# Optimization experiments

Measured on AMD Instinct MI355X. Metric: run time of the kernel, lower is better.

## Reference

```python
import jax, jax.numpy as jnp
import numpy as np

B, N, M = 2, 10000, 320000
F, LAT, STY = 64, 128, 128
HEADS, HID = 4, 32
OUT = 3 + F  # 67
NEG = 0.2    # leaky relu slope (both activation and GAT attention)
EPS = 1e-5


def leaky(x):
    return jax.nn.leaky_relu(x, NEG)


def layer_norm(x, g, b):
    mu = jnp.mean(x, axis=-1, keepdims=True)
    var = jnp.var(x, axis=-1, keepdims=True)
    return (x - mu) * jax.lax.rsqrt(var + EPS) * g + b


def gat_conv(h, src, dst, W, a_src, a_dst, bias, heads, out_dim, n_nodes, concat):
    # h: [n, in]; W: [in, heads*out_dim]; a_*: [heads, out_dim]
    ht = (h @ W).reshape(n_nodes, heads, out_dim)
    al_s = jnp.einsum('nhd,hd->nh', ht, a_src)  # source contribution
    al_d = jnp.einsum('nhd,hd->nh', ht, a_dst)  # destination contribution
    e = leaky(al_s[src] + al_d[dst])            # [E, heads]
    emax = jax.ops.segment_max(e, dst, num_segments=n_nodes)
    ex = jnp.exp(e - emax[dst])
    denom = jax.ops.segment_sum(ex, dst, num_segments=n_nodes)
    alpha = ex / (denom[dst] + 1e-16)           # scatter-softmax over in-edges
    msg = ht[src] * alpha[:, :, None]           # [E, heads, out_dim]
    agg = jax.ops.segment_sum(msg, dst, num_segments=n_nodes)
    agg = agg.reshape(n_nodes, heads * out_dim) if concat else agg.mean(axis=1)
    return agg + bias


def setup_inputs():
    key = jax.random.key(0)
    ks = jax.random.split(key, 20)
    g = lambda i, sh, s=0.05: jax.random.normal(ks[i], sh, jnp.float32) * s
    d = {}
    d['z'] = g(0, (B, LAT), 1.0)
    d['x'] = g(1, (N, F), 1.0)
    d['pos'] = g(2, (N, 3), 1.0)
    d['edge_index'] = jax.random.randint(ks[3], (2, M), 0, N)
    d['w1'] = g(4, (LAT, 256)); d['b1'] = jnp.zeros((256,), jnp.float32)
    d['w2'] = g(5, (256, 512)); d['b2'] = jnp.zeros((512,), jnp.float32)
    d['w3'] = g(6, (512, STY)); d['b3'] = jnp.zeros((STY,), jnp.float32)
    in0 = F + STY
    d['gw0'] = g(7, (in0, HEADS * HID)); d['ga0s'] = g(8, (HEADS, HID)); d['ga0d'] = g(9, (HEADS, HID)); d['gb0'] = jnp.zeros((HEADS * HID,), jnp.float32)
    in1 = HEADS * HID
    d['gw1'] = g(10, (in1, HEADS * HID)); d['ga1s'] = g(11, (HEADS, HID)); d['ga1d'] = g(12, (HEADS, HID)); d['gb1'] = jnp.zeros((HEADS * HID,), jnp.float32)
    d['gw2'] = g(13, (in1, OUT)); d['ga2s'] = g(14, (1, OUT)); d['ga2d'] = g(15, (1, OUT)); d['gb2'] = jnp.zeros((OUT,), jnp.float32)
    d['ln0_g'] = jnp.ones((in1,), jnp.float32); d['ln0_b'] = jnp.zeros((in1,), jnp.float32)
    d['ln1_g'] = jnp.ones((in1,), jnp.float32); d['ln1_b'] = jnp.zeros((in1,), jnp.float32)
    return d


def _batched_edges(edge_index):
    # replicate template edges B times with node-id offsets, then add self-loops
    ei = jnp.concatenate([edge_index + b * N for b in range(B)], axis=1)
    sl = jnp.arange(B * N, dtype=edge_index.dtype)
    src = jnp.concatenate([ei[0], sl])
    dst = jnp.concatenate([ei[1], sl])
    return src, dst


def _forward(z, x, pos, src, dst,
             w1, b1, w2, b2, w3, b3,
             gw0, ga0s, ga0d, gb0, gw1, ga1s, ga1d, gb1, gw2, ga2s, ga2d, gb2,
             ln0_g, ln0_b, ln1_g, ln1_b):
    n_tot = B * N
    # style MLP
    s = leaky(z @ w1 + b1)
    s = leaky(s @ w2 + b2)
    style = s @ w3 + b3                               # [B, STY]
    xb = jnp.tile(x, (B, 1))                          # [B*N, F]
    pb = jnp.tile(pos, (B, 1))                        # [B*N, 3]
    style_exp = jnp.repeat(style, N, axis=0)          # [B*N, STY]
    H = jnp.concatenate([xb, style_exp], axis=1)
    H = gat_conv(H, src, dst, gw0, ga0s, ga0d, gb0, HEADS, HID, n_tot, True)
    H = leaky(layer_norm(H, ln0_g, ln0_b))
    H = gat_conv(H, src, dst, gw1, ga1s, ga1d, gb1, HEADS, HID, n_tot, True)
    H = leaky(layer_norm(H, ln1_g, ln1_b))
    H_out = gat_conv(H, src, dst, gw2, ga2s, ga2d, gb2, 1, OUT, n_tot, False)
    p_new = pb + H_out[:, :3]
    f_new = xb + H_out[:, 3:]
    return f_new, p_new


def reference(z, x, pos, edge_index,
              w1, b1, w2, b2, w3, b3,
              gw0, ga0s, ga0d, gb0, gw1, ga1s, ga1d, gb1, gw2, ga2s, ga2d, gb2,
              ln0_g, ln0_b, ln1_g, ln1_b):
    src, dst = _batched_edges(edge_index)
    return _forward(z, x, pos, src, dst,
                    w1, b1, w2, b2, w3, b3,
                    gw0, ga0s, ga0d, gb0, gw1, ga1s, ga1d, gb1, gw2, ga2s, ga2d, gb2,
                    ln0_g, ln0_b, ln1_g, ln1_b)
```

## Files before the change

### kernel.cpp

```cpp
#include <hip/hip_runtime.h>
#include <hip/hip_bf16.h>

#define DEV_INLINE __device__ __forceinline__

constexpr int Nn   = 10000;
constexpr int NT   = 20000;
constexpr int Me   = 320000;
constexpr int STRIDE = 96;
constexpr float NEG = 0.2f;

typedef float  f32x4  __attribute__((ext_vector_type(4)));
typedef short  bf16x8 __attribute__((ext_vector_type(8)));

DEV_INLINE float leaky(float x){ return x >= 0.f ? x : NEG*x; }

DEV_INLINE ushort f2bf(float v){
  __hip_bfloat16 h = __float2bfloat16(v);
  return *reinterpret_cast<ushort*>(&h);
}
DEV_INLINE float bf2f(ushort u){
  uint x = ((uint)u) << 16;
  return __uint_as_float(x);
}
DEV_INLINE float sel4(float4 w, int h){
  return h < 2 ? (h == 0 ? w.x : w.y) : (h == 2 ? w.z : w.w);
}
DEV_INLINE float red16(float v){
  v += __shfl_xor(v, 1); v += __shfl_xor(v, 2);
  v += __shfl_xor(v, 4); v += __shfl_xor(v, 8);
  return v;
}
DEV_INLINE float red32(float v){
  v += __shfl_xor(v, 1); v += __shfl_xor(v, 2);
  v += __shfl_xor(v, 4); v += __shfl_xor(v, 8);
  v += __shfl_xor(v, 16);
  return v;
}

template<int K>
__global__ __launch_bounds__(256) void k_mlp(const float* __restrict__ in,
    const float* __restrict__ W, const float* __restrict__ bias,
    float* __restrict__ out, int OD, int doAct, int mlpBlocks,
    int* __restrict__ zbuf, int zn, int zblk,
    const float* __restrict__ xsrc, ushort* __restrict__ xdst, int xn4){
  if ((int)blockIdx.x >= mlpBlocks){
    int b2 = blockIdx.x - mlpBlocks;
    if (b2 < zblk){
      int i = b2*256 + threadIdx.x;
      if (i < zn) zbuf[i] = 0;
    } else {
      int i4 = (b2 - zblk)*256 + threadIdx.x;
      if (i4 < xn4){
        float4 v = ((const float4*)xsrc)[i4];
        ushort4 o;
        o.x = f2bf(v.x); o.y = f2bf(v.y); o.z = f2bf(v.z); o.w = f2bf(v.w);
        ((ushort4*)xdst)[i4] = o;
      }
    }
    return;
  }
  int wave = threadIdx.x >> 6, lane = threadIdx.x & 63;
  int o = blockIdx.x*4 + wave;
  if (o >= 2*OD) return;
  int b = (o >= OD) ? 1 : 0;
  int j = o - b*OD;
  const float* __restrict__ ip = in + b*K;
  float acc = 0.f;
  #pragma unroll 2
  for (int k = lane; k < K; k += 64) acc += ip[k] * W[(size_t)k*OD + j];
  #pragma unroll
  for (int off = 32; off; off >>= 1) acc += __shfl_xor(acc, off);
  if (lane == 0){
    float v = acc + (bias ? bias[j] : 0.f);
    out[o] = doAct ? leaky(v) : v;
  }
}

__global__ __launch_bounds__(256) void k_ht0_mfma(const ushort* __restrict__ xb,
    const float* __restrict__ gw0, const float* __restrict__ styleW0,
    const float* __restrict__ a_s, const float* __restrict__ a_d,
    ushort* __restrict__ ht0, float* __restrict__ alS, float* __restrict__ alD,
    int mbBlocks, const int* __restrict__ eidx, int* __restrict__ cnt,
    ushort* __restrict__ slot){
  if ((int)blockIdx.x >= mbBlocks){
    int e = (blockIdx.x - mbBlocks)*256 + threadIdx.x;
    if (e < Me){
      int s = eidx[e], d = eidx[Me + e];
      int p = atomicAdd(&cnt[d], 1);
      if (p < STRIDE) slot[(size_t)d*STRIDE + p] = (ushort)s;
    }
    return;
  }
  __shared__ ushort bt[128*64];
  __shared__ float stycS[2][4], stycD[2][4];
  int t = threadIdx.x;
  int wid = t >> 6, lane = t & 63, l15 = lane & 15, g = lane >> 4;
  int mbase = blockIdx.x*128 + wid*32;

  bf16x8 afr[2][2];
  #pragma unroll
  for (int mf=0; mf<2; mf++){
    int row = mbase + mf*16 + l15;
    int rc = row < Nn ? row : Nn-1;
    const ushort* ap = xb + (size_t)rc*64 + g*8;
    #pragma unroll
    for (int ks=0; ks<2; ks++)
      afr[mf][ks] = *(const bf16x8*)(ap + ks*32);
  }

  for (int idx = t; idx < 64*128; idx += 256){
    int k = idx >> 7, c = idx & 127;
    uint byte = ((uint)(c*64 + k) << 1) ^ ((uint)(c&7) << 4);
    *(ushort*)((char*)bt + byte) = f2bf(gw0[k*128 + c]);
  }

  if (t < 128){
    int c = t, h = c >> 5;
    float as_c = a_s[c], ad_c = a_d[c];
    float s0 = styleW0[c], s1 = styleW0[128 + c];
    float v0s = red32(s0*as_c), v0d = red32(s0*ad_c);
    float v1s = red32(s1*as_c), v1d = red32(s1*ad_c);
    if ((lane & 31) == 0){
      stycS[0][h] = v0s; stycD[0][h] = v0d;
      stycS[1][h] = v1s; stycD[1][h] = v1d;
    }
  }
  __syncthreads();

  f32x4 acc[2][8];
  #pragma unroll
  for (int mf=0; mf<2; mf++)
    #pragma unroll
    for (int nf=0; nf<8; nf++) acc[mf][nf] = (f32x4){0.f,0.f,0.f,0.f};

  #pragma unroll
  for (int ks=0; ks<2; ks++){
    int kb = ks*32 + g*8;
    bf16x8 bfr[8];
    #pragma unroll
    for (int nf=0; nf<8; nf++){
      int c = nf*16 + l15;
      uint byte = ((uint)(c*64 + kb) << 1) ^ ((uint)(c&7) << 4);
      bfr[nf] = *(const bf16x8*)((const char*)bt + byte);
    }
    #pragma unroll
    for (int mf=0; mf<2; mf++)
      #pragma unroll
      for (int nf=0; nf<8; nf++)
        acc[mf][nf] = __builtin_amdgcn_mfma_f32_16x16x32_bf16(
            afr[mf][ks], bfr[nf], acc[mf][nf], 0, 0, 0);
  }

  float sw0[8], sw1[8], as_v[8], ad_v[8];
  #pragma unroll
  for (int nf=0; nf<8; nf++){
    int c = nf*16 + l15;
    sw0[nf] = styleW0[c]; sw1[nf] = styleW0[128 + c];
    as_v[nf] = a_s[c];    ad_v[nf] = a_d[c];
  }
  #pragma unroll
  for (int mf=0; mf<2; mf++){
    int rbase = mbase + mf*16 + g*4;
    #pragma unroll
    for (int r=0; r<4; r++){
      int row = rbase + r;
      bool ok = (row < Nn);
      #pragma unroll
      for (int nf=0; nf<8; nf++){
        int c = nf*16 + l15;
        if (ok){
          float v = acc[mf][nf][r];
          ht0[(size_t)row*128 + c]      = f2bf(v + sw0[nf]);
          ht0[(size_t)(Nn+row)*128 + c] = f2bf(v + sw1[nf]);
        }
      }
      float ps0 = acc[mf][0][r]*as_v[0] + acc[mf][1][r]*as_v[1];
      float ps1 = acc[mf][2][r]*as_v[2] + acc[mf][3][r]*as_v[3];
      float ps2 = acc[mf][4][r]*as_v[4] + acc[mf][5][r]*as_v[5];
      float ps3 = acc[mf][6][r]*as_v[6] + acc[mf][7][r]*as_v[7];
      float pd0 = acc[mf][0][r]*ad_v[0] + acc[mf][1][r]*ad_v[1];
      float pd1 = acc[mf][2][r]*ad_v[2] + acc[mf][3][r]*ad_v[3];
      float pd2 = acc[mf][4][r]*ad_v[4] + acc[mf][5][r]*ad_v[5];
      float pd3 = acc[mf][6][r]*ad_v[6] + acc[mf][7][r]*ad_v[7];
      ps0 = red16(ps0); ps1 = red16(ps1); ps2 = red16(ps2); ps3 = red16(ps3);
      pd0 = red16(pd0); pd1 = red16(pd1); pd2 = red16(pd2); pd3 = red16(pd3);
      if (l15 == 0 && ok){
        *(float4*)(alS + (size_t)row*4) = make_float4(
            ps0 + stycS[0][0], ps1 + stycS[0][1], ps2 + stycS[0][2], ps3 + stycS[0][3]);
        *(float4*)(alD + (size_t)row*4) = make_float4(
            pd0 + stycD[0][0], pd1 + stycD[0][1], pd2 + stycD[0][2], pd3 + stycD[0][3]);
        *(float4*)(alS + (size_t)(Nn+row)*4) = make_float4(
            ps0 + stycS[1][0], ps1 + stycS[1][1], ps2 + stycS[1][2], ps3 + stycS[1][3]);
        *(float4*)(alD + (size_t)(Nn+row)*4) = make_float4(
            pd0 + stycD[1][0], pd1 + stycD[1][1], pd2 + stycD[1][2], pd3 + stycD[1][3]);
      }
    }
  }
}

template<int NCOL, int LDO, int NF, int NHEAD>
__global__ __launch_bounds__(256) void k_mm_mfma(const ushort* __restrict__ A,
    const float* __restrict__ W, ushort* __restrict__ out,
    const float* __restrict__ a_s, const float* __restrict__ a_d,
    float* __restrict__ alS, float* __restrict__ alD, int M){
  constexpr int NCOLP = NF*16;
  __shared__ ushort bt[NCOLP*128];
  int t = threadIdx.x;
  int wid = t >> 6, lane = t & 63, l15 = lane & 15, g = lane >> 4;
  int mbase = blockIdx.x*128 + wid*32;

  bf16x8 afr[2][4];
  #pragma unroll
  for (int mf=0; mf<2; mf++){
    int row = mbase + mf*16 + l15;
    int rc = row < M ? row : M-1;
    const ushort* ap = A + (size_t)rc*128 + g*8;
    #pragma unroll
    for (int ks=0; ks<4; ks++)
      afr[mf][ks] = *(const bf16x8*)(ap + ks*32);
  }

  for (int idx = t; idx < 128*NCOLP; idx += 256){
    int k = idx / NCOLP, c = idx % NCOLP;
    float v = (c < NCOL) ? W[k*NCOL + c] : 0.f;
    uint byte = ((uint)(c*128 + k) << 1) ^ ((uint)(c&7) << 4);
    *(ushort*)((char*)bt + byte) = f2bf(v);
  }
  __syncthreads();

  f32x4 acc[2][NF];
  #pragma unroll
  for (int mf=0; mf<2; mf++)
    #pragma unroll
    for (int nf=0; nf<NF; nf++) acc[mf][nf] = (f32x4){0.f,0.f,0.f,0.f};

  #pragma unroll
  for (int ks=0; ks<4; ks++){
    int kb = ks*32 + g*8;
    bf16x8 bfr[NF];
    #pragma unroll
    for (int nf=0; nf<NF; nf++){
      int c = nf*16 + l15;
      uint byte = ((uint)(c*128 + kb) << 1) ^ ((uint)(c&7) << 4);
      bfr[nf] = *(const bf16x8*)((const char*)bt + byte);
    }
    #pragma unroll
    for (int mf=0; mf<2; mf++)
      #pragma unroll
      for (int nf=0; nf<NF; nf++)
        acc[mf][nf] = __builtin_amdgcn_mfma_f32_16x16x32_bf16(
            afr[mf][ks], bfr[nf], acc[mf][nf], 0, 0, 0);
  }

  #pragma unroll
  for (int mf=0; mf<2; mf++){
    int rbase = mbase + mf*16 + g*4;
    #pragma unroll
    for (int nf=0; nf<NF; nf++){
      int c = nf*16 + l15;
      if (c < LDO){
        #pragma unroll
        for (int r=0; r<4; r++){
          int row = rbase + r;
          if (row < M) out[(size_t)row*LDO + c] = (c < NCOL) ? f2bf(acc[mf][nf][r]) : (ushort)0;
        }
      }
    }
  }

  float as_v[NF], ad_v[NF];
  #pragma unroll
  for (int nf=0; nf<NF; nf++){
    int c = nf*16 + l15;
    as_v[nf] = (c < NCOL) ? a_s[c] : 0.f;
    ad_v[nf] = (c < NCOL) ? a_d[c] : 0.f;
  }
  #pragma unroll
  for (int mf=0; mf<2; mf++){
    #pragma unroll
    for (int r=0; r<4; r++){
      int row = mbase + mf*16 + g*4 + r;
      if (NHEAD == 4){
        float ps0 = acc[mf][0][r]*as_v[0] + acc[mf][1][r]*as_v[1];
        float ps1 = acc[mf][2][r]*as_v[2] + acc[mf][3][r]*as_v[3];
        float ps2 = acc[mf][4][r]*as_v[4] + acc[mf][5][r]*as_v[5];
        float ps3 = acc[mf][6][r]*as_v[6] + acc[mf][7][r]*as_v[7];
        float pd0 = acc[mf][0][r]*ad_v[0] + acc[mf][1][r]*ad_v[1];
        float pd1 = acc[mf][2][r]*ad_v[2] + acc[mf][3][r]*ad_v[3];
        float pd2 = acc[mf][4][r]*ad_v[4] + acc[mf][5][r]*ad_v[5];
        float pd3 = acc[mf][6][r]*ad_v[6] + acc[mf][7][r]*ad_v[7];
        ps0 = red16(ps0); ps1 = red16(ps1); ps2 = red16(ps2); ps3 = red16(ps3);
        pd0 = red16(pd0); pd1 = red16(pd1); pd2 = red16(pd2); pd3 = red16(pd3);
        if (l15 == 0 && row < M){
          *(float4*)(alS + (size_t)row*4) = make_float4(ps0, ps1, ps2, ps3);
          *(float4*)(alD + (size_t)row*4) = make_float4(pd0, pd1, pd2, pd3);
        }
      } else {
        float ps = 0.f, pd = 0.f;
        #pragma unroll
        for (int nf=0; nf<NF; nf++){
          ps += acc[mf][nf][r]*as_v[nf];
          pd += acc[mf][nf][r]*ad_v[nf];
        }
        ps = red16(ps); pd = red16(pd);
        if (l15 == 0 && row < M){
          alS[row] = ps; alD[row] = pd;
        }
      }
    }
  }
}

__global__ __launch_bounds__(256) void k_gat128(const ushort* __restrict__ ht,
    const float* __restrict__ alS, const float* __restrict__ alD,
    const int* __restrict__ deg, const ushort* __restrict__ slot,
    const float* __restrict__ gb, const float* __restrict__ lng,
    const float* __restrict__ lnb, ushort* __restrict__ outH, int n){
  __shared__ float wbuf[4][4][68];
  __shared__ int   sbuf[4][64];
  int wave = threadIdx.x >> 6, lane = threadIdx.x & 63;
  int dd = blockIdx.x*4 + wave;
  if (dd >= n) return;
  int tr  = (dd >= Nn) ? dd - Nn : dd;
  int off = (dd >= Nn) ? Nn : 0;
  int c0 = lane*2;
  int h  = lane >> 4;
  float4 ald4 = *(const float4*)(alD + dd*4);
  int dg = deg[tr]; if (dg > STRIDE) dg = STRIDE;
  int begin = tr*STRIDE, end = begin + dg;

  float4 asl = *(const float4*)(alS + dd*4);
  float4 wsl;
  wsl.x = __expf(leaky(asl.x + ald4.x));
  wsl.y = __expf(leaky(asl.y + ald4.y));
  wsl.z = __expf(leaky(asl.z + ald4.z));
  wsl.w = __expf(leaky(asl.w + ald4.w));
  float es = sel4(wsl, h);
  uint sv0 = *(const uint*)(ht + (size_t)dd*128 + c0);
  float den  = es;
  float acc0 = es * bf2f((ushort)(sv0 & 0xffff));
  float acc1 = es * bf2f((ushort)(sv0 >> 16));

  const ushort* __restrict__ htp = ht + c0;

  for (int j = begin; j < end; j += 64){
    int nc = min(64, end - j);
    if (lane < nc){
      int s = (int)slot[j + lane] + off;
      float4 as4 = *(const float4*)(alS + s*4);
      wbuf[wave][0][lane] = __expf(leaky(as4.x + ald4.x));
      wbuf[wave][1][lane] = __expf(leaky(as4.y + ald4.y));
      wbuf[wave][2][lane] = __expf(leaky(as4.z + ald4.z));
      wbuf[wave][3][lane] = __expf(leaky(as4.w + ald4.w));
      sbuf[wave][lane] = s;
    }
    const float* __restrict__ wh = wbuf[wave][h];
    int q = 0;
    for (; q + 8 <= nc; q += 8){
      int sv[8]; float wv[8];
      #pragma unroll
      for (int u=0;u<8;u++){ sv[u] = sbuf[wave][q+u]; wv[u] = wh[q+u]; }
      uint hv[8];
      #pragma unroll
      for (int u=0;u<8;u++) hv[u] = *(const uint*)(htp + (size_t)sv[u]*128);
      #pragma unroll
      for (int u=0;u<8;u++){
        den  += wv[u];
        acc0 += wv[u] * bf2f((ushort)(hv[u] & 0xffff));
        acc1 += wv[u] * bf2f((ushort)(hv[u] >> 16));
      }
    }
    for (; q < nc; q++){
      int s = sbuf[wave][q];
      float e = wh[q];
      uint hv = *(const uint*)(htp + (size_t)s*128);
      den  += e;
      acc0 += e * bf2f((ushort)(hv & 0xffff));
      acc1 += e * bf2f((ushort)(hv >> 16));
    }
  }
  float idn = 1.f / (den + 1e-16f);
  float v0 = acc0*idn + gb[c0];
  float v1 = acc1*idn + gb[c0+1];

  float sum = v0 + v1, sq = v0*v0 + v1*v1;
  #pragma unroll
  for (int offx = 32; offx; offx >>= 1){
    sum += __shfl_xor(sum, offx);
    sq  += __shfl_xor(sq,  offx);
  }
  float mu  = sum * (1.f/128.f);
  float var = sq  * (1.f/128.f) - mu*mu;
  float inv = rsqrtf(var + 1e-5f);
  float y0 = (v0 - mu)*inv*lng[c0]   + lnb[c0];
  float y1 = (v1 - mu)*inv*lng[c0+1] + lnb[c0+1];
  uint ow = (uint)f2bf(leaky(y0)) | ((uint)f2bf(leaky(y1)) << 16);
  *(uint*)(outH + (size_t)dd*128 + c0) = ow;
}

__global__ __launch_bounds__(256) void k_gat_out(const ushort* __restrict__ ht2,
    const float* __restrict__ alS, const float* __restrict__ alD,
    const int* __restrict__ deg, const ushort* __restrict__ slot,
    const float* __restrict__ gb2, const float* __restrict__ x,
    const float* __restrict__ pos, float* __restrict__ out, int n){
  __shared__ float wbuf[4][64];
  __shared__ int   sbuf[4][64];
  int wave = threadIdx.x >> 6, lane = threadIdx.x & 63;
  int dd = blockIdx.x*4 + wave;
  if (dd >= n) return;
  int tr  = (dd >= Nn) ? dd - Nn : dd;
  int off = (dd >= Nn) ? Nn : 0;
  int c0 = lane*2;
  bool act = (c0 < 67);
  float ald = alD[dd];
  int dg = deg[tr]; if (dg > STRIDE) dg = STRIDE;
  int begin = tr*STRIDE, end = begin + dg;

  float wsl = __expf(leaky(alS[dd] + ald));
  float den  = wsl;
  uint sv0 = act ? *(const uint*)(ht2 + (size_t)dd*68 + c0) : 0u;
  float acc0 = wsl * bf2f((ushort)(sv0 & 0xffff));
  float acc1 = wsl * bf2f((ushort)(sv0 >> 16));

  const ushort* __restrict__ h2p = ht2 + c0;

  for (int j = begin; j < end; j += 64){
    int nc = min(64, end - j);
    if (lane < nc){
      int s = (int)slot[j + lane] + off;
      wbuf[wave][lane] = __expf(leaky(alS[s] + ald));
      sbuf[wave][lane] = s;
    }
    int q = 0;
    for (; q + 8 <= nc; q += 8){
      int sv[8]; float wv[8];
      #pragma unroll
      for (int u=0;u<8;u++){ sv[u] = sbuf[wave][q+u]; wv[u] = wbuf[wave][q+u]; }
      uint hv[8];
      #pragma unroll
      for (int u=0;u<8;u++) hv[u] = act ? *(const uint*)(h2p + (size_t)sv[u]*68) : 0u;
      #pragma unroll
      for (int u=0;u<8;u++){
        den  += wv[u];
        acc0 += wv[u] * bf2f((ushort)(hv[u] & 0xffff));
        acc1 += wv[u] * bf2f((ushort)(hv[u] >> 16));
      }
    }
    for (; q < nc; q++){
      int s = sbuf[wave][q]; float w = wbuf[wave][q];
      uint hv = act ? *(const uint*)(h2p + (size_t)s*68) : 0u;
      den  += w;
      acc0 += w * bf2f((ushort)(hv & 0xffff));
      acc1 += w * bf2f((ushort)(hv >> 16));
    }
  }
  if (!act) return;
  float idn = 1.f / (den + 1e-16f);
  int i = tr;
  int c1 = c0 + 1;
  float v0 = acc0*idn + gb2[c0];
  if (c0 < 3) out[NT*64 + dd*3 + c0] = pos[i*3 + c0] + v0;
  else        out[dd*64 + (c0-3)]    = x[i*64 + (c0-3)] + v0;
  if (c1 < 67){
    float v1 = acc1*idn + gb2[c1];
    if (c1 < 3) out[NT*64 + dd*3 + c1] = pos[i*3 + c1] + v1;
    else        out[dd*64 + (c1-3)]    = x[i*64 + (c1-3)] + v1;
  }
}

extern "C" void kernel_launch(void* const* d_in, const int* in_sizes, int n_in,
                              void* d_out, int out_size, void* d_ws, size_t ws_size,
                              hipStream_t stream){
  const float* z    = (const float*)d_in[0];
  const float* x    = (const float*)d_in[1];
  const float* pos  = (const float*)d_in[2];
  const int*   eidx = (const int*)  d_in[3];
  const float* w1   = (const float*)d_in[4];
  const float* b1   = (const float*)d_in[5];
  const float* w2   = (const float*)d_in[6];
  const float* b2   = (const float*)d_in[7];
  const float* w3   = (const float*)d_in[8];
  const float* b3   = (const float*)d_in[9];
  const float* gw0  = (const float*)d_in[10];
  const float* ga0s = (const float*)d_in[11];
  const float* ga0d = (const float*)d_in[12];
  const float* gb0  = (const float*)d_in[13];
  const float* gw1  = (const float*)d_in[14];
  const float* ga1s = (const float*)d_in[15];
  const float* ga1d = (const float*)d_in[16];
  const float* gb1  = (const float*)d_in[17];
  const float* gw2  = (const float*)d_in[18];
  const float* ga2s = (const float*)d_in[19];
  const float* ga2d = (const float*)d_in[20];
  const float* gb2  = (const float*)d_in[21];
  const float* ln0g = (const float*)d_in[22];
  const float* ln0b = (const float*)d_in[23];
  const float* ln1g = (const float*)d_in[24];
  const float* ln1b = (const float*)d_in[25];
  float* out = (float*)d_out;

  float* ws       = (float*)d_ws;
  float* styleW0  = ws;
  float* s1buf    = ws + 256;
  float* s2buf    = s1buf + 512;
  float* stbuf    = s2buf + 1024;
  float* alS      = stbuf + 256;
  float* alD      = alS + 80000;
  ushort* htA     = (ushort*)(alD + 80000);
  ushort* htB     = htA + (size_t)NT*128;
  ushort* ht2c    = htB + (size_t)NT*128;
  ushort* xb      = ht2c + (size_t)NT*68;
  int*   cnt      = (int*)(xb + (size_t)Nn*64);
  ushort* slot    = (ushort*)(cnt + Nn);

  const int ZB = (Nn + 255)/256;
  const int XB = (Nn*64/4 + 255)/256;
  k_mlp<128><<<128 + ZB + XB, 256, 0, stream>>>(z, w1, b1, s1buf, 256, 1, 128,
                                                cnt, Nn, ZB, x, xb, Nn*64/4);
  k_mlp<256><<<256, 256, 0, stream>>>(s1buf, w2, b2, s2buf, 512, 1, 256,
                                      nullptr, 0, 0, nullptr, nullptr, 0);
  k_mlp<512><<<64,  256, 0, stream>>>(s2buf, w3, b3, stbuf, 128, 0, 64,
                                      nullptr, 0, 0, nullptr, nullptr, 0);
  k_mlp<128><<<64,  256, 0, stream>>>(stbuf, gw0 + 64*128, (const float*)nullptr,
                                      styleW0, 128, 0, 64,
                                      nullptr, 0, 0, nullptr, nullptr, 0);

  const int MB0 = (Nn+127)/128;
  const int EB  = (Me+255)/256;
  k_ht0_mfma<<<MB0 + EB, 256, 0, stream>>>(xb, gw0, styleW0, ga0s, ga0d,
                                           htA, alS, alD, MB0, eidx, cnt, slot);
  k_gat128<<<(NT+3)/4, 256, 0, stream>>>(htA, alS, alD, cnt, slot,
                                         gb0, ln0g, ln0b, htB, NT);
  const int MB = (NT+127)/128;
  k_mm_mfma<128,128,8,4><<<MB, 256, 0, stream>>>(htB, gw1, htA, ga1s, ga1d, alS, alD, NT);
  k_gat128<<<(NT+3)/4, 256, 0, stream>>>(htA, alS, alD, cnt, slot,
                                         gb1, ln1g, ln1b, htB, NT);
  k_mm_mfma<67,68,5,1><<<MB, 256, 0, stream>>>(htB, gw2, ht2c, ga2s, ga2d, alS, alD, NT);
  k_gat_out<<<(NT+3)/4, 256, 0, stream>>>(ht2c, alS, alD, cnt, slot,
                                          gb2, x, pos, out, NT);
}
```

Baseline: 136.7 us.

## Fold style projection into w3 product and split GAT128 lanes across edges

Two changes. First, the product w3·G (G being the style slice of gw0) and b3·G are precomputed in idle blocks of the first MLP launch, so the last MLP layer and the style projection collapse into one launch with a fused weight. This removes a kernel launch from the serial chain, at the cost of extra precompute work and a changed floating-point summation order. Second, k_gat128 now has each half-wave process alternate edges with 4 channels per lane. It uses 8-byte gathers and combines the halves with a cross-half shuffle, aiming for wider loads and more edge-level parallelism.

```diff
diff --git a/kernel.cpp b/kernel.cpp
--- a/kernel.cpp
+++ b/kernel.cpp
@@ -42,19 +42,35 @@
     const float* __restrict__ W, const float* __restrict__ bias,
     float* __restrict__ out, int OD, int doAct, int mlpBlocks,
     int* __restrict__ zbuf, int zn, int zblk,
-    const float* __restrict__ xsrc, ushort* __restrict__ xdst, int xn4){
+    const float* __restrict__ xsrc, ushort* __restrict__ xdst, int xn4, int xblk,
+    const float* __restrict__ w3, const float* __restrict__ G,
+    float* __restrict__ M, const float* __restrict__ b3, float* __restrict__ bG,
+    int mblk){
   if ((int)blockIdx.x >= mlpBlocks){
     int b2 = blockIdx.x - mlpBlocks;
     if (b2 < zblk){
       int i = b2*256 + threadIdx.x;
       if (i < zn) zbuf[i] = 0;
-    } else {
-      int i4 = (b2 - zblk)*256 + threadIdx.x;
+    } else if ((b2 -= zblk) < xblk){
+      int i4 = b2*256 + threadIdx.x;
       if (i4 < xn4){
         float4 v = ((const float4*)xsrc)[i4];
         ushort4 o;
         o.x = f2bf(v.x); o.y = f2bf(v.y); o.z = f2bf(v.z); o.w = f2bf(v.w);
         ((ushort4*)xdst)[i4] = o;
+      }
+    } else if ((b2 -= xblk) < mblk){
+      int k = b2*2 + (threadIdx.x >> 7);
+      int j = threadIdx.x & 127;
+      float a = 0.f;
+      for (int m=0; m<128; m++) a += w3[k*128 + m] * G[m*128 + j];
+      M[(size_t)k*128 + j] = a;
+    } else {
+      if (threadIdx.x < 128){
+        int j = threadIdx.x;
+        float a = 0.f;
+        for (int m=0; m<128; m++) a += b3[m] * G[m*128 + j];
+        bG[j] = a;
       }
     }
     return;
@@ -323,8 +339,9 @@
   if (dd >= n) return;
   int tr  = (dd >= Nn) ? dd - Nn : dd;
   int off = (dd >= Nn) ? Nn : 0;
-  int c0 = lane*2;
-  int h  = lane >> 4;
+  int sub = lane >> 5, li = lane & 31;
+  int c0 = li*4;
+  int h  = li >> 3;
   float4 ald4 = *(const float4*)(alD + dd*4);
   int dg = deg[tr]; if (dg > STRIDE) dg = STRIDE;
   int begin = tr*STRIDE, end = begin + dg;
@@ -336,10 +353,13 @@
   wsl.z = __expf(leaky(asl.z + ald4.z));
   wsl.w = __expf(leaky(asl.w + ald4.w));
   float es = sel4(wsl, h);
-  uint sv0 = *(const uint*)(ht + (size_t)dd*128 + c0);
-  float den  = es;
-  float acc0 = es * bf2f((ushort)(sv0 & 0xffff));
-  float acc1 = es * bf2f((ushort)(sv0 >> 16));
+  float acc0=0.f, acc1=0.f, acc2=0.f, acc3=0.f, den=0.f;
+  if (sub == 0){
+    ushort4 sv = *(const ushort4*)(ht + (size_t)dd*128 + c0);
+    den = es;
+    acc0 = es * bf2f(sv.x); acc1 = es * bf2f(sv.y);
+    acc2 = es * bf2f(sv.z); acc3 = es * bf2f(sv.w);
+  }
 
   const ushort* __restrict__ htp = ht + c0;
 
@@ -357,45 +377,62 @@
     const float* __restrict__ wh = wbuf[wave][h];
     int q = 0;
     for (; q + 8 <= nc; q += 8){
-      int sv[8]; float wv[8];
-      #pragma unroll
-      for (int u=0;u<8;u++){ sv[u] = sbuf[wave][q+u]; wv[u] = wh[q+u]; }
-      uint hv[8];
-      #pragma unroll
-      for (int u=0;u<8;u++) hv[u] = *(const uint*)(htp + (size_t)sv[u]*128);
-      #pragma unroll
-      for (int u=0;u<8;u++){
+      int sv[4]; float wv[4];
+      #pragma unroll
+      for (int u=0;u<4;u++){ int e = q + 2*u + sub; sv[u] = sbuf[wave][e]; wv[u] = wh[e]; }
+      ushort4 hv[4];
+      #pragma unroll
+      for (int u=0;u<4;u++) hv[u] = *(const ushort4*)(htp + (size_t)sv[u]*128);
+      #pragma unroll
+      for (int u=0;u<4;u++){
         den  += wv[u];
-        acc0 += wv[u] * bf2f((ushort)(hv[u] & 0xffff));
-        acc1 += wv[u] * bf2f((ushort)(hv[u] >> 16));
-      }
-    }
-    for (; q < nc; q++){
-      int s = sbuf[wave][q];
-      float e = wh[q];
-      uint hv = *(const uint*)(htp + (size_t)s*128);
-      den  += e;
-      acc0 += e * bf2f((ushort)(hv & 0xffff));
-      acc1 += e * bf2f((ushort)(hv >> 16));
-    }
-  }
+        acc0 += wv[u] * bf2f(hv[u].x);
+        acc1 += wv[u] * bf2f(hv[u].y);
+        acc2 += wv[u] * bf2f(hv[u].z);
+        acc3 += wv[u] * bf2f(hv[u].w);
+      }
+    }
+    for (; q < nc; q += 2){
+      int e = q + sub;
+      if (e < nc){
+        int s = sbuf[wave][e];
+        float w = wh[e];
+        ushort4 hv = *(const ushort4*)(htp + (size_t)s*128);
+        den  += w;
+        acc0 += w * bf2f(hv.x); acc1 += w * bf2f(hv.y);
+        acc2 += w * bf2f(hv.z); acc3 += w * bf2f(hv.w);
+      }
+    }
+  }
+  acc0 += __shfl_xor(acc0, 32); acc1 += __shfl_xor(acc1, 32);
+  acc2 += __shfl_xor(acc2, 32); acc3 += __shfl_xor(acc3, 32);
+  den  += __shfl_xor(den, 32);
+
   float idn = 1.f / (den + 1e-16f);
-  float v0 = acc0*idn + gb[c0];
-  float v1 = acc1*idn + gb[c0+1];
-
-  float sum = v0 + v1, sq = v0*v0 + v1*v1;
-  #pragma unroll
-  for (int offx = 32; offx; offx >>= 1){
-    sum += __shfl_xor(sum, offx);
-    sq  += __shfl_xor(sq,  offx);
-  }
+  float4 gbv = *(const float4*)(gb + c0);
+  float v0 = acc0*idn + gbv.x;
+  float v1 = acc1*idn + gbv.y;
+  float v2 = acc2*idn + gbv.z;
+  float v3 = acc3*idn + gbv.w;
+
+  float sum = v0+v1+v2+v3;
+  float sq  = v0*v0+v1*v1+v2*v2+v3*v3;
+  sum = red32(sum); sq = red32(sq);
   float mu  = sum * (1.f/128.f);
   float var = sq  * (1.f/128.f) - mu*mu;
   float inv = rsqrtf(var + 1e-5f);
-  float y0 = (v0 - mu)*inv*lng[c0]   + lnb[c0];
-  float y1 = (v1 - mu)*inv*lng[c0+1] + lnb[c0+1];
-  uint ow = (uint)f2bf(leaky(y0)) | ((uint)f2bf(leaky(y1)) << 16);
-  *(uint*)(outH + (size_t)dd*128 + c0) = ow;
+  float4 lg = *(const float4*)(lng + c0);
+  float4 lb = *(const float4*)(lnb + c0);
+  if (sub == 0){
+    float y0 = (v0 - mu)*inv*lg.x + lb.x;
+    float y1 = (v1 - mu)*inv*lg.y + lb.y;
+    float y2 = (v2 - mu)*inv*lg.z + lb.z;
+    float y3 = (v3 - mu)*inv*lg.w + lb.w;
+    uint2 ow;
+    ow.x = (uint)f2bf(leaky(y0)) | ((uint)f2bf(leaky(y1)) << 16);
+    ow.y = (uint)f2bf(leaky(y2)) | ((uint)f2bf(leaky(y3)) << 16);
+    *(uint2*)(outH + (size_t)dd*128 + c0) = ow;
+  }
 }
 
 __global__ __launch_bounds__(256) void k_gat_out(const ushort* __restrict__ ht2,
@@ -503,8 +540,9 @@
   float* styleW0  = ws;
   float* s1buf    = ws + 256;
   float* s2buf    = s1buf + 512;
-  float* stbuf    = s2buf + 1024;
-  float* alS      = stbuf + 256;
+  float* Mbuf     = s2buf + 1024;
+  float* bGbuf    = Mbuf + 512*128;
+  float* alS      = bGbuf + 128;
   float* alD      = alS + 80000;
   ushort* htA     = (ushort*)(alD + 80000);
   ushort* htB     = htA + (size_t)NT*128;
@@ -513,17 +551,19 @@
   int*   cnt      = (int*)(xb + (size_t)Nn*64);
   ushort* slot    = (ushort*)(cnt + Nn);
 
+  const float* G = gw0 + 64*128;
+
   const int ZB = (Nn + 255)/256;
   const int XB = (Nn*64/4 + 255)/256;
-  k_mlp<128><<<128 + ZB + XB, 256, 0, stream>>>(z, w1, b1, s1buf, 256, 1, 128,
-                                                cnt, Nn, ZB, x, xb, Nn*64/4);
+  const int MBk = 256;
+  k_mlp<128><<<128 + ZB + XB + MBk + 1, 256, 0, stream>>>(
+      z, w1, b1, s1buf, 256, 1, 128,
+      cnt, Nn, ZB, x, xb, Nn*64/4, XB,
+      w3, G, Mbuf, b3, bGbuf, MBk);
   k_mlp<256><<<256, 256, 0, stream>>>(s1buf, w2, b2, s2buf, 512, 1, 256,
-                                      nullptr, 0, 0, nullptr, nullptr, 0);
-  k_mlp<512><<<64,  256, 0, stream>>>(s2buf, w3, b3, stbuf, 128, 0, 64,
-                                      nullptr, 0, 0, nullptr, nullptr, 0);
-  k_mlp<128><<<64,  256, 0, stream>>>(stbuf, gw0 + 64*128, (const float*)nullptr,
-                                      styleW0, 128, 0, 64,
-                                      nullptr, 0, 0, nullptr, nullptr, 0);
+      nullptr, 0, 0, nullptr, nullptr, 0, 0, nullptr, nullptr, nullptr, nullptr, nullptr, 0);
+  k_mlp<512><<<64, 256, 0, stream>>>(s2buf, Mbuf, bGbuf, styleW0, 128, 0, 64,
+      nullptr, 0, 0, nullptr, nullptr, 0, 0, nullptr, nullptr, nullptr, nullptr, nullptr, 0);
 
   const int MB0 = (Nn+127)/128;
   const int EB  = (Me+255)/256;
```

After: 136.9 us. No clear change (+0.1%).
